# Kernel optimization log

Hardware: AMD Instinct MI355X
Metric: run time of the kernel (lower is better)

## Reference

```python
import jax, jax.numpy as jnp
import numpy as np

NL = 256
NP = 8192
NV = 16
B = 2


def _xavier(key, shape):
    fan_in, fan_out = shape[-2], shape[-1]
    lim = np.sqrt(6.0 / (fan_in + fan_out))
    return jax.random.uniform(key, shape, jnp.float32, -lim, lim)


def setup_inputs() -> dict:
    key = jax.random.key(0)
    ks = jax.random.split(key, 12)
    return {
        "nodes": jax.random.normal(ks[0], (B, NP, NL), jnp.float32),
        "edges_attributes": jax.random.normal(ks[1], (NP, NV, NL), jnp.float32),
        "edges_indices": jax.random.randint(ks[2], (NP, NV), 0, NP, jnp.int64) if jax.config.jax_enable_x64 else jax.random.randint(ks[2], (NP, NV), 0, NP).astype(jnp.int32),
        # edge MLP (dim_in=3*NL, nb_hidden=3 -> first + 2 hidden + last)
        "e_fw": _xavier(ks[3], (3 * NL, NL)), "e_fb": jnp.zeros((NL,), jnp.float32),
        "e_hw": _xavier(ks[4], (2, NL, NL)), "e_hb": jnp.zeros((2, NL), jnp.float32),
        "e_lw": _xavier(ks[5], (NL, NL)), "e_lb": jnp.zeros((NL,), jnp.float32),
        # node MLP (dim_in=2*NL)
        "n_fw": _xavier(ks[6], (2 * NL, NL)), "n_fb": jnp.zeros((NL,), jnp.float32),
        "n_hw": _xavier(ks[7], (2, NL, NL)), "n_hb": jnp.zeros((2, NL), jnp.float32),
        "n_lw": _xavier(ks[8], (NL, NL)), "n_lb": jnp.zeros((NL,), jnp.float32),
    }


def _mlp(x, fw, fb, hw, hb, lw, lb):
    x = jax.nn.relu(x @ fw + fb)
    for i in range(hw.shape[0]):  # fixed small number of hidden layers
        x = jax.nn.relu(x @ hw[i] + hb[i])
    return x @ lw + lb


def reference(nodes, edges_attributes, edges_indices,
              e_fw, e_fb, e_hw, e_hb, e_lw, e_lb,
              n_fw, n_fb, n_hw, n_hb, n_lw, n_lb):
    b, npts, nl = nodes.shape
    nv = edges_indices.shape[1]
    # gather neighbor features: [B, Np, Nv, Nl]
    nodes_nb = jnp.take(nodes, edges_indices, axis=1)
    # self features broadcast over neighbor axis, edge attrs broadcast over batch
    self_exp = jnp.broadcast_to(nodes[:, :, None, :], (b, npts, nv, nl))
    edge_exp = jnp.broadcast_to(edges_attributes[None], (b, npts, nv, nl))
    concat_msg = jnp.concatenate([self_exp, nodes_nb, edge_exp], axis=-1)  # [B,Np,Nv,3Nl]
    new_edges = _mlp(concat_msg, e_fw, e_fb, e_hw, e_hb, e_lw, e_lb)  # [B,Np,Nv,Nl]
    agg = jnp.sum(new_edges, axis=2)  # [B,Np,Nl]
    concat_nodes = jnp.concatenate([nodes, agg], axis=-1)  # [B,Np,2Nl]
    new_nodes = nodes + _mlp(concat_nodes, n_fw, n_fb, n_hw, n_hb, n_lw, n_lb)
    return new_nodes, new_edges[0]
```

## Files before the change

### kernel.cpp

```cpp
#include <hip/hip_runtime.h>
#include <hip/hip_bf16.h>


typedef __bf16 bf16;
typedef __bf16 bf16x8 __attribute__((ext_vector_type(8)));
typedef float f32x4 __attribute__((ext_vector_type(4)));

#define MFMA16(a, b, c) __builtin_amdgcn_mfma_f32_16x16x32_bf16((a), (b), (c), 0, 0, 0)

constexpr int kNP = 8192;
constexpr int kNV = 16;

__global__ void pack_w(const float* __restrict__ src, bf16* __restrict__ dst,
                       int kd, int N) {
  int t = blockIdx.x * 256 + threadIdx.x;
  int j = t & 7;
  int l = (t >> 3) & 63;
  int r2 = t >> 9;
  int ks = r2 % kd;
  int nt = r2 / kd;
  int k = ks * 32 + ((l >> 4) << 3) + j;
  int n = (nt << 4) + (l & 15);
  dst[t] = (bf16)src[k * N + n];
}

template <int KD, int MT>
__device__ __forceinline__ void layer_acc(const bf16* X, int xs,
                                          const bf16* __restrict__ Wp,
                                          const float* __restrict__ bias,
                                          f32x4 (&acc)[MT][4]) {
  const int lane = threadIdx.x & 63;
  const int w = threadIdx.x >> 6;
  const int q = lane >> 4;
  const int c = lane & 15;
#pragma unroll
  for (int nt = 0; nt < 4; nt++) {
    float bv = bias ? bias[w * 64 + nt * 16 + c] : 0.0f;
#pragma unroll
    for (int mt = 0; mt < MT; mt++) {
      acc[mt][nt][0] = bv;
      acc[mt][nt][1] = bv;
      acc[mt][nt][2] = bv;
      acc[mt][nt][3] = bv;
    }
  }
#pragma unroll
  for (int ks = 0; ks < KD; ks++) {
    bf16x8 a[MT];
#pragma unroll
    for (int mt = 0; mt < MT; mt++)
      a[mt] = *(const bf16x8*)(X + (mt * 16 + c) * xs + ks * 32 + q * 8);
    bf16x8 bb[4];
#pragma unroll
    for (int nt = 0; nt < 4; nt++)
      bb[nt] = *(const bf16x8*)(Wp + ((((w * 4 + nt) * KD + ks) * 64 + lane) << 3));
#pragma unroll
    for (int mt = 0; mt < MT; mt++)
#pragma unroll
      for (int nt = 0; nt < 4; nt++)
        acc[mt][nt] = MFMA16(a[mt], bb[nt], acc[mt][nt]);
  }
}

template <int KD, int MT, bool RELU>
__device__ __forceinline__ void layer_inplace(bf16* X, int xs_r, int xs_w,
                                              const bf16* __restrict__ Wp,
                                              const float* __restrict__ bias) {
  f32x4 acc[MT][4];
  layer_acc<KD, MT>(X, xs_r, Wp, bias, acc);
  const int lane = threadIdx.x & 63;
  const int w = threadIdx.x >> 6;
  const int q = lane >> 4;
  const int c = lane & 15;
  __syncthreads();
#pragma unroll
  for (int mt = 0; mt < MT; mt++)
#pragma unroll
    for (int nt = 0; nt < 4; nt++)
#pragma unroll
      for (int i = 0; i < 4; i++) {
        float v = acc[mt][nt][i];
        if (RELU) v = fmaxf(v, 0.0f);
        X[(mt * 16 + q * 4 + i) * xs_w + (w * 64 + nt * 16 + c)] = (bf16)v;
      }
  __syncthreads();
}

__global__ __launch_bounds__(256) void gemm_fp32in(
    const float* __restrict__ A, const bf16* __restrict__ Wp,
    const float* __restrict__ bias, bf16* __restrict__ out) {
  __shared__ bf16 X[64 * 280];
  const int t = threadIdx.x;
  const int r = t >> 2;
  const int q4 = t & 3;
  const int m = blockIdx.x * 64 + r;
  const float* Arow = A + m * 256 + q4 * 64;
  bf16* Xrow = X + r * 280 + q4 * 64;
#pragma unroll
  for (int c8 = 0; c8 < 8; c8++) {
    float4 f0 = *(const float4*)(Arow + c8 * 8);
    float4 f1 = *(const float4*)(Arow + c8 * 8 + 4);
    bf16x8 v;
    v[0] = (bf16)f0.x; v[1] = (bf16)f0.y; v[2] = (bf16)f0.z; v[3] = (bf16)f0.w;
    v[4] = (bf16)f1.x; v[5] = (bf16)f1.y; v[6] = (bf16)f1.z; v[7] = (bf16)f1.w;
    *(bf16x8*)(Xrow + c8 * 8) = v;
  }
  __syncthreads();
  layer_inplace<8, 4, false>(X, 280, 280, Wp, bias);
  bf16* orow = out + m * 256 + q4 * 64;
#pragma unroll
  for (int c8 = 0; c8 < 8; c8++)
    *(uint4*)(orow + c8 * 8) = *(const uint4*)(Xrow + c8 * 8);
}

__global__ __launch_bounds__(256) void edge_mlp(
    const bf16* __restrict__ S, const bf16* __restrict__ P,
    const bf16* __restrict__ E, const int* __restrict__ idx,
    const bf16* __restrict__ Wh0, const bf16* __restrict__ Wh1,
    const bf16* __restrict__ Wl, const float* __restrict__ e_hb,
    const float* __restrict__ e_lb, bf16* __restrict__ agg,
    float* __restrict__ out_edges) {
  __shared__ bf16 X[64 * 280];
  const int t = threadIdx.x;
  const int e0 = blockIdx.x * 64;
  const int b = e0 >> 17;
  const int pbase = (e0 >> 4) & (kNP - 1);
  {
    const int r = t >> 2;
    const int q4 = t & 3;
    const int p = pbase + (r >> 4);
    const int v = r & 15;
    const int nb = idx[p * kNV + v];
    const bf16* Srow = S + ((b << 13) + p) * 256 + q4 * 64;
    const bf16* Prow = P + ((b << 13) + nb) * 256 + q4 * 64;
    const bf16* Erow = E + (p * kNV + v) * 256 + q4 * 64;
    bf16* Xrow = X + r * 280 + q4 * 64;
#pragma unroll
    for (int c8 = 0; c8 < 8; c8++) {
      bf16x8 sv = *(const bf16x8*)(Srow + c8 * 8);
      bf16x8 pv = *(const bf16x8*)(Prow + c8 * 8);
      bf16x8 ev = *(const bf16x8*)(Erow + c8 * 8);
      bf16x8 o;
#pragma unroll
      for (int j = 0; j < 8; j++) {
        float f = (float)sv[j] + (float)pv[j] + (float)ev[j];
        o[j] = (bf16)fmaxf(f, 0.0f);
      }
      *(bf16x8*)(Xrow + c8 * 8) = o;
    }
  }
  __syncthreads();
  layer_inplace<8, 4, true>(X, 280, 280, Wh0, e_hb);
  layer_inplace<8, 4, true>(X, 280, 280, Wh1, e_hb + 256);
  f32x4 acc[4][4];
  layer_acc<8, 4>(X, 280, Wl, e_lb, acc);
  const int lane = t & 63;
  const int w = t >> 6;
  const int q = lane >> 4;
  const int c = lane & 15;
#pragma unroll
  for (int mt = 0; mt < 4; mt++) {
#pragma unroll
    for (int nt = 0; nt < 4; nt++) {
      float s = acc[mt][nt][0] + acc[mt][nt][1] + acc[mt][nt][2] + acc[mt][nt][3];
      s += __shfl_xor(s, 16, 64);
      s += __shfl_xor(s, 32, 64);
      if (lane < 16)
        agg[((b << 13) + pbase + mt) * 256 + w * 64 + nt * 16 + lane] = (bf16)s;
    }
  }
  if (b == 0) {
#pragma unroll
    for (int mt = 0; mt < 4; mt++)
#pragma unroll
      for (int nt = 0; nt < 4; nt++)
#pragma unroll
        for (int i = 0; i < 4; i++) {
          int e = e0 + mt * 16 + q * 4 + i;
          out_edges[e * 256 + (w * 64 + nt * 16 + c)] = acc[mt][nt][i];
        }
  }
}

__global__ __launch_bounds__(256) void node_mlp(
    const float* __restrict__ nodes, const bf16* __restrict__ agg,
    const bf16* __restrict__ Wf, const bf16* __restrict__ Wh0,
    const bf16* __restrict__ Wh1, const bf16* __restrict__ Wl,
    const float* __restrict__ n_fb, const float* __restrict__ n_hb,
    const float* __restrict__ n_lb, float* __restrict__ out_nodes) {
  __shared__ bf16 X[32 * 536];
  const int t = threadIdx.x;
  const int r = t >> 3;
  const int q8 = t & 7;
  const int m = blockIdx.x * 32 + r;
  bf16* Xrow = X + r * 536;
  const float* Arow = nodes + m * 256 + q8 * 32;
#pragma unroll
  for (int c8 = 0; c8 < 4; c8++) {
    float4 f0 = *(const float4*)(Arow + c8 * 8);
    float4 f1 = *(const float4*)(Arow + c8 * 8 + 4);
    bf16x8 v;
    v[0] = (bf16)f0.x; v[1] = (bf16)f0.y; v[2] = (bf16)f0.z; v[3] = (bf16)f0.w;
    v[4] = (bf16)f1.x; v[5] = (bf16)f1.y; v[6] = (bf16)f1.z; v[7] = (bf16)f1.w;
    *(bf16x8*)(Xrow + q8 * 32 + c8 * 8) = v;
  }
  const bf16* Grow = agg + m * 256 + q8 * 32;
#pragma unroll
  for (int c8 = 0; c8 < 4; c8++)
    *(bf16x8*)(Xrow + 256 + q8 * 32 + c8 * 8) = *(const bf16x8*)(Grow + c8 * 8);
  __syncthreads();
  layer_inplace<16, 2, true>(X, 536, 280, Wf, n_fb);
  layer_inplace<8, 2, true>(X, 280, 280, Wh0, n_hb);
  layer_inplace<8, 2, true>(X, 280, 280, Wh1, n_hb + 256);
  f32x4 acc[2][4];
  layer_acc<8, 2>(X, 280, Wl, n_lb, acc);
  const int lane = t & 63;
  const int w = t >> 6;
  const int q = lane >> 4;
  const int c = lane & 15;
#pragma unroll
  for (int mt = 0; mt < 2; mt++)
#pragma unroll
    for (int nt = 0; nt < 4; nt++)
#pragma unroll
      for (int i = 0; i < 4; i++) {
        int mm = blockIdx.x * 32 + mt * 16 + q * 4 + i;
        int col = w * 64 + nt * 16 + c;
        out_nodes[mm * 256 + col] = nodes[mm * 256 + col] + acc[mt][nt][i];
      }
}

extern "C" void kernel_launch(void* const* d_in, const int* in_sizes, int n_in,
                              void* d_out, int out_size, void* d_ws,
                              size_t ws_size, hipStream_t stream) {
  const float* nodes = (const float*)d_in[0];
  const float* eattr = (const float*)d_in[1];
  const int* eidx = (const int*)d_in[2];
  const float* e_fw = (const float*)d_in[3];
  const float* e_fb = (const float*)d_in[4];
  const float* e_hw = (const float*)d_in[5];
  const float* e_hb = (const float*)d_in[6];
  const float* e_lw = (const float*)d_in[7];
  const float* e_lb = (const float*)d_in[8];
  const float* n_fw = (const float*)d_in[9];
  const float* n_fb = (const float*)d_in[10];
  const float* n_hw = (const float*)d_in[11];
  const float* n_hb = (const float*)d_in[12];
  const float* n_lw = (const float*)d_in[13];
  const float* n_lb = (const float*)d_in[14];

  char* ws = (char*)d_ws;
  bf16* Sb = (bf16*)(ws + 0);
  bf16* Pb = (bf16*)(ws + 8388608);
  bf16* Eb = (bf16*)(ws + 16777216);
  bf16* aggb = (bf16*)(ws + 83886080);
  bf16* wp = (bf16*)(ws + 92274688);
  bf16* w_self = wp;
  bf16* w_nb = wp + 65536;
  bf16* w_ea = wp + 131072;
  bf16* w_eh0 = wp + 196608;
  bf16* w_eh1 = wp + 262144;
  bf16* w_el = wp + 327680;
  bf16* w_nf = wp + 393216;
  bf16* w_nh0 = wp + 524288;
  bf16* w_nh1 = wp + 589824;
  bf16* w_nl = wp + 655360;

  float* out_nodes = (float*)d_out;
  float* out_edges = (float*)d_out + 4194304;

  pack_w<<<256, 256, 0, stream>>>(e_fw, w_self, 8, 256);
  pack_w<<<256, 256, 0, stream>>>(e_fw + 65536, w_nb, 8, 256);
  pack_w<<<256, 256, 0, stream>>>(e_fw + 131072, w_ea, 8, 256);
  pack_w<<<256, 256, 0, stream>>>(e_hw, w_eh0, 8, 256);
  pack_w<<<256, 256, 0, stream>>>(e_hw + 65536, w_eh1, 8, 256);
  pack_w<<<256, 256, 0, stream>>>(e_lw, w_el, 8, 256);
  pack_w<<<512, 256, 0, stream>>>(n_fw, w_nf, 16, 256);
  pack_w<<<256, 256, 0, stream>>>(n_hw, w_nh0, 8, 256);
  pack_w<<<256, 256, 0, stream>>>(n_hw + 65536, w_nh1, 8, 256);
  pack_w<<<256, 256, 0, stream>>>(n_lw, w_nl, 8, 256);

  gemm_fp32in<<<256, 256, 0, stream>>>(nodes, w_self, e_fb, Sb);
  gemm_fp32in<<<256, 256, 0, stream>>>(nodes, w_nb, nullptr, Pb);
  gemm_fp32in<<<2048, 256, 0, stream>>>(eattr, w_ea, nullptr, Eb);

  edge_mlp<<<4096, 256, 0, stream>>>(Sb, Pb, Eb, eidx, w_eh0, w_eh1, w_el,
                                     e_hb, e_lb, aggb, out_edges);
  node_mlp<<<512, 256, 0, stream>>>(nodes, aggb, w_nf, w_nh0, w_nh1, w_nl,
                                    n_fb, n_hb, n_lb, out_nodes);
}
```

Before: 555.5 us.

## Merge weight-pack and producer GEMM launches; use 512-thread blocks splitting rows across waves

Merges the ten weight-packing launches into a single kernel and the three producer GEMMs into a single launch. Doubles block size to 512 threads in all MLP kernels, with the extra four waves taking the other half of the rows in each tile, and adds launch_bounds occupancy hints. The aim is to cut launch overhead and raise the wave count per CU. In exchange, each wave does fewer MFMAs per weight fragment load, which lowers B-operand reuse, and the larger blocks may change register limits.

```diff
diff --git a/kernel.cpp b/kernel.cpp
--- a/kernel.cpp
+++ b/kernel.cpp
@@ -11,37 +11,49 @@
 constexpr int kNP = 8192;
 constexpr int kNV = 16;
 
-__global__ void pack_w(const float* __restrict__ src, bf16* __restrict__ dst,
-                       int kd, int N) {
+__global__ __launch_bounds__(256) void pack_all(
+    const float* __restrict__ e_fw, const float* __restrict__ e_hw,
+    const float* __restrict__ e_lw, const float* __restrict__ n_fw,
+    const float* __restrict__ n_hw, const float* __restrict__ n_lw,
+    bf16* __restrict__ wp) {
   int t = blockIdx.x * 256 + threadIdx.x;
-  int j = t & 7;
-  int l = (t >> 3) & 63;
-  int r2 = t >> 9;
+  const float* src;
+  int kd = 8, local;
+  if (t < 196608) {
+    src = e_fw + (t >> 16) * 65536; local = t & 65535;
+  } else if (t < 262144) { src = e_hw;           local = t - 196608;
+  } else if (t < 327680) { src = e_hw + 65536;   local = t - 262144;
+  } else if (t < 393216) { src = e_lw;           local = t - 327680;
+  } else if (t < 524288) { src = n_fw;           local = t - 393216; kd = 16;
+  } else if (t < 589824) { src = n_hw;           local = t - 524288;
+  } else if (t < 655360) { src = n_hw + 65536;   local = t - 589824;
+  } else               { src = n_lw;             local = t - 655360; }
+  int j = local & 7;
+  int l = (local >> 3) & 63;
+  int r2 = local >> 9;
   int ks = r2 % kd;
   int nt = r2 / kd;
   int k = ks * 32 + ((l >> 4) << 3) + j;
   int n = (nt << 4) + (l & 15);
-  dst[t] = (bf16)src[k * N + n];
+  wp[t] = (bf16)src[k * 256 + n];
 }
 
 template <int KD, int MT>
 __device__ __forceinline__ void layer_acc(const bf16* X, int xs,
                                           const bf16* __restrict__ Wp,
                                           const float* __restrict__ bias,
-                                          f32x4 (&acc)[MT][4]) {
+                                          f32x4 (&acc)[MT][4], int rowOff,
+                                          int wc) {
   const int lane = threadIdx.x & 63;
-  const int w = threadIdx.x >> 6;
   const int q = lane >> 4;
   const int c = lane & 15;
 #pragma unroll
   for (int nt = 0; nt < 4; nt++) {
-    float bv = bias ? bias[w * 64 + nt * 16 + c] : 0.0f;
+    float bv = bias ? bias[wc * 64 + nt * 16 + c] : 0.0f;
 #pragma unroll
     for (int mt = 0; mt < MT; mt++) {
-      acc[mt][nt][0] = bv;
-      acc[mt][nt][1] = bv;
-      acc[mt][nt][2] = bv;
-      acc[mt][nt][3] = bv;
+      acc[mt][nt][0] = bv; acc[mt][nt][1] = bv;
+      acc[mt][nt][2] = bv; acc[mt][nt][3] = bv;
     }
   }
 #pragma unroll
@@ -49,11 +61,11 @@
     bf16x8 a[MT];
 #pragma unroll
     for (int mt = 0; mt < MT; mt++)
-      a[mt] = *(const bf16x8*)(X + (mt * 16 + c) * xs + ks * 32 + q * 8);
+      a[mt] = *(const bf16x8*)(X + (rowOff + mt * 16 + c) * xs + ks * 32 + q * 8);
     bf16x8 bb[4];
 #pragma unroll
     for (int nt = 0; nt < 4; nt++)
-      bb[nt] = *(const bf16x8*)(Wp + ((((w * 4 + nt) * KD + ks) * 64 + lane) << 3));
+      bb[nt] = *(const bf16x8*)(Wp + ((((wc * 4 + nt) * KD + ks) * 64 + lane) << 3));
 #pragma unroll
     for (int mt = 0; mt < MT; mt++)
 #pragma unroll
@@ -65,11 +77,11 @@
 template <int KD, int MT, bool RELU>
 __device__ __forceinline__ void layer_inplace(bf16* X, int xs_r, int xs_w,
                                               const bf16* __restrict__ Wp,
-                                              const float* __restrict__ bias) {
+                                              const float* __restrict__ bias,
+                                              int rowOff, int wc) {
   f32x4 acc[MT][4];
-  layer_acc<KD, MT>(X, xs_r, Wp, bias, acc);
+  layer_acc<KD, MT>(X, xs_r, Wp, bias, acc, rowOff, wc);
   const int lane = threadIdx.x & 63;
-  const int w = threadIdx.x >> 6;
   const int q = lane >> 4;
   const int c = lane & 15;
   __syncthreads();
@@ -81,39 +93,46 @@
       for (int i = 0; i < 4; i++) {
         float v = acc[mt][nt][i];
         if (RELU) v = fmaxf(v, 0.0f);
-        X[(mt * 16 + q * 4 + i) * xs_w + (w * 64 + nt * 16 + c)] = (bf16)v;
+        X[(rowOff + mt * 16 + q * 4 + i) * xs_w + (wc * 64 + nt * 16 + c)] = (bf16)v;
       }
   __syncthreads();
 }
 
-__global__ __launch_bounds__(256) void gemm_fp32in(
-    const float* __restrict__ A, const bf16* __restrict__ Wp,
-    const float* __restrict__ bias, bf16* __restrict__ out) {
+__global__ __launch_bounds__(512, 4) void producer_gemm(
+    const float* __restrict__ nodes, const float* __restrict__ eattr,
+    const bf16* __restrict__ w_self, const bf16* __restrict__ w_nb,
+    const bf16* __restrict__ w_ea, const float* __restrict__ e_fb,
+    bf16* __restrict__ Sb, bf16* __restrict__ Pb, bf16* __restrict__ Eb) {
   __shared__ bf16 X[64 * 280];
   const int t = threadIdx.x;
-  const int r = t >> 2;
-  const int q4 = t & 3;
-  const int m = blockIdx.x * 64 + r;
-  const float* Arow = A + m * 256 + q4 * 64;
-  bf16* Xrow = X + r * 280 + q4 * 64;
-#pragma unroll
-  for (int c8 = 0; c8 < 8; c8++) {
-    float4 f0 = *(const float4*)(Arow + c8 * 8);
-    float4 f1 = *(const float4*)(Arow + c8 * 8 + 4);
+  const int m0 = blockIdx.x * 64;
+  const float* A; const float* bias = nullptr; const bf16* Wp; bf16* out;
+  if (m0 < 16384)      { A = nodes + m0 * 256;           Wp = w_self; bias = e_fb; out = Sb + m0 * 256; }
+  else if (m0 < 32768) { A = nodes + (m0 - 16384) * 256; Wp = w_nb;   out = Pb + (m0 - 16384) * 256; }
+  else                 { A = eattr + (m0 - 32768) * 256; Wp = w_ea;   out = Eb + (m0 - 32768) * 256; }
+  const int r = t >> 3;
+  const int q8 = t & 7;
+#pragma unroll
+  for (int c8 = 0; c8 < 4; c8++) {
+    int col = q8 * 8 + c8 * 64;
+    float4 f0 = *(const float4*)(A + r * 256 + col);
+    float4 f1 = *(const float4*)(A + r * 256 + col + 4);
     bf16x8 v;
     v[0] = (bf16)f0.x; v[1] = (bf16)f0.y; v[2] = (bf16)f0.z; v[3] = (bf16)f0.w;
     v[4] = (bf16)f1.x; v[5] = (bf16)f1.y; v[6] = (bf16)f1.z; v[7] = (bf16)f1.w;
-    *(bf16x8*)(Xrow + c8 * 8) = v;
-  }
-  __syncthreads();
-  layer_inplace<8, 4, false>(X, 280, 280, Wp, bias);
-  bf16* orow = out + m * 256 + q4 * 64;
-#pragma unroll
-  for (int c8 = 0; c8 < 8; c8++)
-    *(uint4*)(orow + c8 * 8) = *(const uint4*)(Xrow + c8 * 8);
-}
-
-__global__ __launch_bounds__(256) void edge_mlp(
+    *(bf16x8*)(X + r * 280 + col) = v;
+  }
+  __syncthreads();
+  const int w = t >> 6;
+  layer_inplace<8, 2, false>(X, 280, 280, Wp, bias, (w >> 2) * 32, w & 3);
+#pragma unroll
+  for (int c8 = 0; c8 < 4; c8++) {
+    int col = q8 * 8 + c8 * 64;
+    *(uint4*)(out + r * 256 + col) = *(const uint4*)(X + r * 280 + col);
+  }
+}
+
+__global__ __launch_bounds__(512, 4) void edge_mlp(
     const bf16* __restrict__ S, const bf16* __restrict__ P,
     const bf16* __restrict__ E, const int* __restrict__ idx,
     const bf16* __restrict__ Wh0, const bf16* __restrict__ Wh1,
@@ -126,63 +145,65 @@
   const int b = e0 >> 17;
   const int pbase = (e0 >> 4) & (kNP - 1);
   {
-    const int r = t >> 2;
-    const int q4 = t & 3;
+    const int r = t >> 3;
+    const int q8 = t & 7;
     const int p = pbase + (r >> 4);
     const int v = r & 15;
     const int nb = idx[p * kNV + v];
-    const bf16* Srow = S + ((b << 13) + p) * 256 + q4 * 64;
-    const bf16* Prow = P + ((b << 13) + nb) * 256 + q4 * 64;
-    const bf16* Erow = E + (p * kNV + v) * 256 + q4 * 64;
-    bf16* Xrow = X + r * 280 + q4 * 64;
-#pragma unroll
-    for (int c8 = 0; c8 < 8; c8++) {
-      bf16x8 sv = *(const bf16x8*)(Srow + c8 * 8);
-      bf16x8 pv = *(const bf16x8*)(Prow + c8 * 8);
-      bf16x8 ev = *(const bf16x8*)(Erow + c8 * 8);
+    const bf16* Srow = S + ((b << 13) + p) * 256;
+    const bf16* Prow = P + ((b << 13) + nb) * 256;
+    const bf16* Erow = E + (p * kNV + v) * 256;
+#pragma unroll
+    for (int c8 = 0; c8 < 4; c8++) {
+      int col = q8 * 8 + c8 * 64;
+      bf16x8 sv = *(const bf16x8*)(Srow + col);
+      bf16x8 pv = *(const bf16x8*)(Prow + col);
+      bf16x8 ev = *(const bf16x8*)(Erow + col);
       bf16x8 o;
 #pragma unroll
       for (int j = 0; j < 8; j++) {
         float f = (float)sv[j] + (float)pv[j] + (float)ev[j];
         o[j] = (bf16)fmaxf(f, 0.0f);
       }
-      *(bf16x8*)(Xrow + c8 * 8) = o;
-    }
-  }
-  __syncthreads();
-  layer_inplace<8, 4, true>(X, 280, 280, Wh0, e_hb);
-  layer_inplace<8, 4, true>(X, 280, 280, Wh1, e_hb + 256);
-  f32x4 acc[4][4];
-  layer_acc<8, 4>(X, 280, Wl, e_lb, acc);
+      *(bf16x8*)(X + r * 280 + col) = o;
+    }
+  }
+  __syncthreads();
+  const int w = t >> 6;
+  const int wc = w & 3;
+  const int rowOff = (w >> 2) * 32;
+  layer_inplace<8, 2, true>(X, 280, 280, Wh0, e_hb, rowOff, wc);
+  layer_inplace<8, 2, true>(X, 280, 280, Wh1, e_hb + 256, rowOff, wc);
+  f32x4 acc[2][4];
+  layer_acc<8, 2>(X, 280, Wl, e_lb, acc, rowOff, wc);
   const int lane = t & 63;
-  const int w = t >> 6;
   const int q = lane >> 4;
   const int c = lane & 15;
 #pragma unroll
-  for (int mt = 0; mt < 4; mt++) {
+  for (int mt = 0; mt < 2; mt++) {
 #pragma unroll
     for (int nt = 0; nt < 4; nt++) {
       float s = acc[mt][nt][0] + acc[mt][nt][1] + acc[mt][nt][2] + acc[mt][nt][3];
       s += __shfl_xor(s, 16, 64);
       s += __shfl_xor(s, 32, 64);
       if (lane < 16)
-        agg[((b << 13) + pbase + mt) * 256 + w * 64 + nt * 16 + lane] = (bf16)s;
+        agg[((b << 13) + pbase + (rowOff >> 4) + mt) * 256 + wc * 64 + nt * 16 + lane] = (bf16)s;
     }
   }
   if (b == 0) {
 #pragma unroll
-    for (int mt = 0; mt < 4; mt++)
+    for (int mt = 0; mt < 2; mt++)
 #pragma unroll
       for (int nt = 0; nt < 4; nt++)
 #pragma unroll
         for (int i = 0; i < 4; i++) {
-          int e = e0 + mt * 16 + q * 4 + i;
-          out_edges[e * 256 + (w * 64 + nt * 16 + c)] = acc[mt][nt][i];
+          int e = e0 + rowOff + mt * 16 + q * 4 + i;
+          out_edges[e * 256 + (wc * 64 + nt * 16 + c)] = acc[mt][nt][i];
         }
   }
 }
 
-__global__ __launch_bounds__(256) void node_mlp(
+__global__ __launch_bounds__(512, 4) void node_mlp(
     const float* __restrict__ nodes, const bf16* __restrict__ agg,
     const bf16* __restrict__ Wf, const bf16* __restrict__ Wh0,
     const bf16* __restrict__ Wh1, const bf16* __restrict__ Wl,
@@ -190,44 +211,44 @@
     const float* __restrict__ n_lb, float* __restrict__ out_nodes) {
   __shared__ bf16 X[32 * 536];
   const int t = threadIdx.x;
-  const int r = t >> 3;
-  const int q8 = t & 7;
+  const int r = t >> 4;
+  const int q16 = t & 15;
   const int m = blockIdx.x * 32 + r;
-  bf16* Xrow = X + r * 536;
-  const float* Arow = nodes + m * 256 + q8 * 32;
 #pragma unroll
   for (int c8 = 0; c8 < 4; c8++) {
-    float4 f0 = *(const float4*)(Arow + c8 * 8);
-    float4 f1 = *(const float4*)(Arow + c8 * 8 + 4);
-    bf16x8 v;
-    v[0] = (bf16)f0.x; v[1] = (bf16)f0.y; v[2] = (bf16)f0.z; v[3] = (bf16)f0.w;
-    v[4] = (bf16)f1.x; v[5] = (bf16)f1.y; v[6] = (bf16)f1.z; v[7] = (bf16)f1.w;
-    *(bf16x8*)(Xrow + q8 * 32 + c8 * 8) = v;
-  }
-  const bf16* Grow = agg + m * 256 + q8 * 32;
-#pragma unroll
-  for (int c8 = 0; c8 < 4; c8++)
-    *(bf16x8*)(Xrow + 256 + q8 * 32 + c8 * 8) = *(const bf16x8*)(Grow + c8 * 8);
-  __syncthreads();
-  layer_inplace<16, 2, true>(X, 536, 280, Wf, n_fb);
-  layer_inplace<8, 2, true>(X, 280, 280, Wh0, n_hb);
-  layer_inplace<8, 2, true>(X, 280, 280, Wh1, n_hb + 256);
-  f32x4 acc[2][4];
-  layer_acc<8, 2>(X, 280, Wl, n_lb, acc);
+    int col = q16 * 8 + c8 * 128;
+    if (col < 256) {
+      float4 f0 = *(const float4*)(nodes + m * 256 + col);
+      float4 f1 = *(const float4*)(nodes + m * 256 + col + 4);
+      bf16x8 v;
+      v[0] = (bf16)f0.x; v[1] = (bf16)f0.y; v[2] = (bf16)f0.z; v[3] = (bf16)f0.w;
+      v[4] = (bf16)f1.x; v[5] = (bf16)f1.y; v[6] = (bf16)f1.z; v[7] = (bf16)f1.w;
+      *(bf16x8*)(X + r * 536 + col) = v;
+    } else {
+      *(bf16x8*)(X + r * 536 + col) =
+          *(const bf16x8*)(agg + m * 256 + (col - 256));
+    }
+  }
+  __syncthreads();
+  const int w = t >> 6;
+  const int wc = w & 3;
+  const int rowOff = (w >> 2) * 16;
+  layer_inplace<16, 1, true>(X, 536, 280, Wf, n_fb, rowOff, wc);
+  layer_inplace<8, 1, true>(X, 280, 280, Wh0, n_hb, rowOff, wc);
+  layer_inplace<8, 1, true>(X, 280, 280, Wh1, n_hb + 256, rowOff, wc);
+  f32x4 acc[1][4];
+  layer_acc<8, 1>(X, 280, Wl, n_lb, acc, rowOff, wc);
   const int lane = t & 63;
-  const int w = t >> 6;
   const int q = lane >> 4;
   const int c = lane & 15;
 #pragma unroll
-  for (int mt = 0; mt < 2; mt++)
-#pragma unroll
-    for (int nt = 0; nt < 4; nt++)
-#pragma unroll
-      for (int i = 0; i < 4; i++) {
-        int mm = blockIdx.x * 32 + mt * 16 + q * 4 + i;
-        int col = w * 64 + nt * 16 + c;
-        out_nodes[mm * 256 + col] = nodes[mm * 256 + col] + acc[mt][nt][i];
-      }
+  for (int nt = 0; nt < 4; nt++)
+#pragma unroll
+    for (int i = 0; i < 4; i++) {
+      int mm = blockIdx.x * 32 + rowOff + q * 4 + i;
+      int col = wc * 64 + nt * 16 + c;
+      out_nodes[mm * 256 + col] = nodes[mm * 256 + col] + acc[0][nt][i];
+    }
 }
 
 extern "C" void kernel_launch(void* const* d_in, const int* in_sizes, int n_in,
@@ -269,23 +290,11 @@
   float* out_nodes = (float*)d_out;
   float* out_edges = (float*)d_out + 4194304;
 
-  pack_w<<<256, 256, 0, stream>>>(e_fw, w_self, 8, 256);
-  pack_w<<<256, 256, 0, stream>>>(e_fw + 65536, w_nb, 8, 256);
-  pack_w<<<256, 256, 0, stream>>>(e_fw + 131072, w_ea, 8, 256);
-  pack_w<<<256, 256, 0, stream>>>(e_hw, w_eh0, 8, 256);
-  pack_w<<<256, 256, 0, stream>>>(e_hw + 65536, w_eh1, 8, 256);
-  pack_w<<<256, 256, 0, stream>>>(e_lw, w_el, 8, 256);
-  pack_w<<<512, 256, 0, stream>>>(n_fw, w_nf, 16, 256);
-  pack_w<<<256, 256, 0, stream>>>(n_hw, w_nh0, 8, 256);
-  pack_w<<<256, 256, 0, stream>>>(n_hw + 65536, w_nh1, 8, 256);
-  pack_w<<<256, 256, 0, stream>>>(n_lw, w_nl, 8, 256);
-
-  gemm_fp32in<<<256, 256, 0, stream>>>(nodes, w_self, e_fb, Sb);
-  gemm_fp32in<<<256, 256, 0, stream>>>(nodes, w_nb, nullptr, Pb);
-  gemm_fp32in<<<2048, 256, 0, stream>>>(eattr, w_ea, nullptr, Eb);
-
-  edge_mlp<<<4096, 256, 0, stream>>>(Sb, Pb, Eb, eidx, w_eh0, w_eh1, w_el,
+  pack_all<<<2816, 256, 0, stream>>>(e_fw, e_hw, e_lw, n_fw, n_hw, n_lw, wp);
+  producer_gemm<<<2560, 512, 0, stream>>>(nodes, eattr, w_self, w_nb, w_ea,
+                                          e_fb, Sb, Pb, Eb);
+  edge_mlp<<<4096, 512, 0, stream>>>(Sb, Pb, Eb, eidx, w_eh0, w_eh1, w_el,
                                      e_hb, e_lb, aggb, out_edges);
-  node_mlp<<<512, 256, 0, stream>>>(nodes, aggb, w_nf, w_nh0, w_nh1, w_nl,
+  node_mlp<<<512, 512, 0, stream>>>(nodes, aggb, w_nf, w_nh0, w_nh1, w_nl,
                                     n_fb, n_hb, n_lb, out_nodes);
 }
```

Measured after the change: 480.9 us. -13.4%, faster.
